# Kernel tuning notes

Measured on AMD Instinct MI355X. Metric: run time of the kernel, lower is better.

## Reference

```python
import jax, jax.numpy as jnp
import numpy as np

INSIZE = 300
OUTSIZE = 300
HSIZE = 300
B, T = 128, 1024


def setup_inputs() -> dict:
    key = jax.random.key(0)
    kx, k1, kb1, k2, kb2 = jax.random.split(key, 5)
    # PyTorch Linear init scale ~ 1/sqrt(fan_in); exact distribution irrelevant for a reference
    s1 = 1.0 / np.sqrt(INSIZE + HSIZE)
    s2 = 1.0 / np.sqrt(HSIZE)
    return {
        "x": jax.random.normal(kx, (B, T, INSIZE), dtype=jnp.float32),
        "W1": jax.random.uniform(k1, (HSIZE, INSIZE + HSIZE), jnp.float32, -s1, s1),
        "b1": jax.random.uniform(kb1, (HSIZE,), jnp.float32, -s1, s1),
        "W2": jax.random.uniform(k2, (OUTSIZE, HSIZE), jnp.float32, -s2, s2),
        "b2": jax.random.uniform(kb2, (OUTSIZE,), jnp.float32, -s2, s2),
    }


def reference(x, W1, b1, W2, b2):
    b = x.shape[0]
    h0 = jnp.zeros((b, HSIZE), dtype=x.dtype)
    # split lin1 weight into input and recurrent parts to avoid per-step concat
    W1x = W1[:, :INSIZE]   # [H, E]
    W1h = W1[:, INSIZE:]   # [H, H]

    def step(h, x_t):
        # h_new = sigmoid(cat([x_t, h]) @ W1.T + b1)
        h_new = jax.nn.sigmoid(x_t @ W1x.T + h @ W1h.T + b1)
        out = h_new @ W2.T + b2
        return h_new, out

    h_final, outs = jax.lax.scan(step, h0, jnp.swapaxes(x, 0, 1))  # outs: [T, B, O]
    return jnp.swapaxes(outs, 0, 1), h_final
```

## Files before the change

### kernel.cpp

```cpp
#include <hip/hip_runtime.h>

typedef __attribute__((ext_vector_type(4))) float f32x4;
typedef __attribute__((ext_vector_type(8))) short bf16x8;

#define B_   128
#define T_   1024
#define NROW 131072
#define HB   (NROW*300)
#define NL2E -1.44269504088896340736f

__device__ inline unsigned short f2bf(float f) {
    union { float f; unsigned int u; } v; v.f = f;
    unsigned int r = v.u + 0x7FFFu + ((v.u >> 16) & 1u);
    return (unsigned short)(r >> 16);
}

__device__ inline uint4 load8_cvt_s(const float* src, bool rowok, int krem, float scale) {
    f32x4 v0 = {0.f,0.f,0.f,0.f}, v1 = {0.f,0.f,0.f,0.f};
    if (rowok) {
        if (krem >= 8)      { v0 = *(const f32x4*)src; v1 = *(const f32x4*)(src + 4); }
        else if (krem >= 4) { v0 = *(const f32x4*)src; }
    }
    v0 *= scale; v1 *= scale;
    uint4 p;
    p.x = (unsigned)f2bf(v0[0]) | ((unsigned)f2bf(v0[1]) << 16);
    p.y = (unsigned)f2bf(v0[2]) | ((unsigned)f2bf(v0[3]) << 16);
    p.z = (unsigned)f2bf(v1[0]) | ((unsigned)f2bf(v1[1]) << 16);
    p.w = (unsigned)f2bf(v1[2]) | ((unsigned)f2bf(v1[3]) << 16);
    return p;
}

__device__ inline uint4 load8_cvt(const float* src, bool rowok, int krem) {
    return load8_cvt_s(src, rowok, krem, 1.0f);
}

__global__ __launch_bounds__(512) void gemm_in_t2(
    const float* __restrict__ X, const float* __restrict__ W1,
    const float* __restrict__ b1, char* __restrict__ aws)
{
    __shared__ unsigned short wlds[19 * 64 * 8];
    __shared__ unsigned short xlds[2][8 * 64 * 8];
    const int tid = threadIdx.x;
    const int w = tid >> 6, l = tid & 63, lg = l >> 4, ln = l & 15;
    const int th = w >> 2, wb = w & 3;
    const int t = blockIdx.x * 2 + th;

    f32x4 acc[2][19];
    #pragma unroll
    for (int q = 0; q < 2; ++q)
        #pragma unroll
        for (int mt = 0; mt < 19; ++mt) acc[q][mt] = (f32x4){0.f,0.f,0.f,0.f};

    for (int kt = 0; kt < 10; ++kt) {
        const int kc = kt * 32;
        __syncthreads();
        #pragma unroll
        for (int rep = 0; rep < 3; ++rep) {
            int e = tid + rep * 512;
            if (e < 1216) {
                int nn = e >> 2, kh = e & 3;
                int k0 = kc + kh * 8;
                uint4 p = load8_cvt_s(W1 + (size_t)nn * 600 + k0, nn < 300, 300 - k0, NL2E);
                *(uint4*)&wlds[(((nn >> 4) * 64) + kh * 16 + (nn & 15)) * 8] = p;
            }
        }
        #pragma unroll
        for (int tt = 0; tt < 2; ++tt) {
            int e = tid;
            int row = e >> 2, kh = e & 3;
            int k0 = kc + kh * 8;
            uint4 p = load8_cvt(X + ((size_t)row * 1024 + blockIdx.x * 2 + tt) * 300 + k0,
                                true, 300 - k0);
            *(uint4*)&xlds[tt][(((row >> 4) * 64) + kh * 16 + (row & 15)) * 8] = p;
        }
        __syncthreads();
        bf16x8 wfr[19];
        #pragma unroll
        for (int mt = 0; mt < 19; ++mt) wfr[mt] = *(const bf16x8*)&wlds[(mt * 64 + l) * 8];
        #pragma unroll
        for (int q = 0; q < 2; ++q) {
            bf16x8 xfr = *(const bf16x8*)&xlds[th][((wb * 2 + q) * 64 + l) * 8];
            #pragma unroll
            for (int mt = 0; mt < 19; ++mt)
                acc[q][mt] = __builtin_amdgcn_mfma_f32_16x16x32_bf16(wfr[mt], xfr, acc[q][mt], 0, 0, 0);
        }
    }

    char* tb = aws + (size_t)t * 76800;
    #pragma unroll
    for (int q = 0; q < 2; ++q) {
        int b = (wb * 2 + q) * 16 + ln;
        #pragma unroll
        for (int mt = 0; mt < 19; ++mt) {
            int rg = mt * 4 + lg;
            if (rg < 75) {
                f32x4 bias = *(const f32x4*)(b1 + mt * 16 + lg * 4);
                float v0 = acc[q][mt][0] + bias[0] * NL2E;
                float v1 = acc[q][mt][1] + bias[1] * NL2E;
                float v2 = acc[q][mt][2] + bias[2] * NL2E;
                float v3 = acc[q][mt][3] + bias[3] * NL2E;
                unsigned plo, phi;
                asm("v_cvt_pk_bf16_f32 %0, %1, %2" : "=v"(plo) : "v"(v0), "v"(v1));
                asm("v_cvt_pk_bf16_f32 %0, %1, %2" : "=v"(phi) : "v"(v2), "v"(v3));
                uint2 pk; pk.x = plo; pk.y = phi;
                *(uint2*)(tb + (size_t)rg * 1024 + b * 8) = pk;
            }
        }
    }
}

#define QOK(q) ((q) < 2 || w4)

#define K2_CHAIN(q)                                                             \
    _Pragma("unroll")                                                           \
    for (int kt = 0; kt < 5; ++kt) {                                            \
        acc[q]  = __builtin_amdgcn_mfma_f32_16x16x32_bf16(afrag[q][kt],   bfr[kt],   acc[q],  0, 0, 0); \
        accB[q] = __builtin_amdgcn_mfma_f32_16x16x32_bf16(afrag[q][kt+5], bfr[kt+5], accB[q], 0, 0, 0); \
    }

#define K2_SIG(q, P, HWT, t)                                                    \
    {                                                                           \
        f32x4 hv;                                                               \
        _Pragma("unroll")                                                       \
        for (int i = 0; i < 4; ++i) {                                           \
            float zn = acc[q][i] + accB[q][i];                  \
            float ex, sg;                                                       \
            asm("v_exp_f32 %0, %1" : "=v"(ex) : "v"(zn));                       \
            asm("v_rcp_f32 %0, %1" : "=v"(sg) : "v"(1.0f + ex));                \
            hv[i] = sg;                                                         \
        }                                                                       \
        unsigned plo, phi;                                                      \
        asm("v_cvt_pk_bf16_f32 %0, %1, %2" : "=v"(plo) : "v"(hv[0]), "v"(hv[1])); \
        asm("v_cvt_pk_bf16_f32 %0, %1, %2" : "=v"(phi) : "v"(hv[2]), "v"(hv[3])); \
        uint2 pk; pk.x = plo; pk.y = phi;                                       \
        *(uint2*)((char*)hlds + ((P) ^ 1) * 10240 + ldsoff[q]) = pk;            \
        if (rq[q] < 300) {                                                      \
            *(uint2*)((HWT) + loff[q]) = pk;         \
            if ((t) == T_ - 1)                                                  \
                *(f32x4*)(hfinal + bb * 300 + rq[q]) = hv;                      \
        }                                                                       \
    }

#define K2W_STEP(P, tval, AS, HWT)                                              \
    {                                                                           \
        const int t = (tval);                                                   \
        bf16x8 bfr[10];                                                         \
        _Pragma("unroll")                                                       \
        for (int kt = 0; kt < 10; ++kt)                                         \
            bfr[kt] = *(const bf16x8*)&hlds[P][(kt * 64 + l) * 8];              \
        f32x4 acc[3], accB[3];                                                  \
        _Pragma("unroll")                                                       \
        for (int q = 0; q < 3; ++q) {                                           \
            union { float f; unsigned u; } u0, u1, u2, u3;                      \
            u0.u = AS[q].x << 16; u1.u = AS[q].x & 0xFFFF0000u;                 \
            u2.u = AS[q].y << 16; u3.u = AS[q].y & 0xFFFF0000u;                 \
            acc[q] = (f32x4){u0.f, u1.f, u2.f, u3.f};                           \
            accB[q] = (f32x4){0.f,0.f,0.f,0.f};                                 \
        }                                                                       \
                        \
        _Pragma("unroll")                                                       \
        for (int q = 0; q < 3; ++q)                                             \
            if (QOK(q)) AS[q] = *(const uint2*)((HWT) + 153600 + loff[q]);      \
        __builtin_amdgcn_s_setprio(1);                                          \
        K2_CHAIN(0)                                                             \
        K2_CHAIN(1)                                                             \
        __builtin_amdgcn_s_setprio(0);                                          \
        K2_SIG(0, P, HWT, t)                                                    \
        if (w4) {                                                               \
            __builtin_amdgcn_s_setprio(1);                                      \
            K2_CHAIN(2)                                                         \
            __builtin_amdgcn_s_setprio(0);                                      \
        }                                                                       \
        K2_SIG(1, P, HWT, t)                                                    \
        if (w4) K2_SIG(2, P, HWT, t)                                            \
        HWT += 153600;                                                          \
        asm volatile("s_waitcnt lgkmcnt(0)" ::: "memory");                      \
        __builtin_amdgcn_s_barrier();                                           \
        asm volatile("" ::: "memory");                                          \
    }

__global__ __launch_bounds__(512) void elman_rec_ws(
    const float* __restrict__ W1, float* __restrict__ hfinal,
    char* __restrict__ hws)
{
    __shared__ unsigned short hlds[2][10 * 64 * 8];
    const int tid = threadIdx.x;
    const int w = tid >> 6, l = tid & 63, lg = l >> 4, ln = l & 15;
    const bool w4 = (w < 4);
    const int bb = blockIdx.x * 16 + ln;

    int rq[3], ldsoff[3], loff[3];
    #pragma unroll
    for (int q = 0; q < 3; ++q) {
        int tile = w4 ? (3 * w + q) : (12 + 2 * (w - 4) + q);
        int r = tile * 16 + 4 * lg;
        rq[q] = r;
        ldsoff[q] = (((r >> 5) * 64 + ((r >> 3) & 3) * 16 + ln) * 8 + (r & 7)) * 2;
        int rgc = r >> 2; if (rgc > 74) rgc = 74;
        loff[q] = rgc * 1024 + bb * 8;
    }

    bf16x8 afrag[3][10];
    #pragma unroll
    for (int q = 0; q < 3; ++q) {
        #pragma unroll
        for (int kt = 0; kt < 10; ++kt) {
            bool qa = (q < 2) || w4;
            int tile = w4 ? (3 * w + q) : (12 + 2 * (w - 4) + q);
            int r = tile * 16 + ln;
            int k0 = kt * 32 + lg * 8;
            uint4 p = load8_cvt_s(W1 + (size_t)r * 600 + 300 + k0,
                                  qa && r < 300, 300 - k0, NL2E);
            union { uint4 u; bf16x8 s; } cv; cv.u = p;
            afrag[q][kt] = cv.s;
        }
    }

    for (int i = tid; i < 10 * 64 * 8; i += 512) hlds[0][i] = 0;

    char* HWT0 = hws;
    char* HWT1 = hws + 76800;

    uint2 AS0[3], AS1[3];
    #pragma unroll
    for (int q = 0; q < 3; ++q)
        if (QOK(q)) {
            AS0[q] = *(const uint2*)(HWT0 + loff[q]);
            AS1[q] = *(const uint2*)(HWT1 + loff[q]);
        }
    __syncthreads();

    for (int t2 = 0; t2 < T_; t2 += 2) {
        K2W_STEP(0, t2,     AS0, HWT0)
        K2W_STEP(1, t2 + 1, AS1, HWT1)
    }
}

__global__ __launch_bounds__(512) void gemm_out_t2(
    const char* __restrict__ hws, const float* __restrict__ W2,
    const float* __restrict__ b2, float* __restrict__ out)
{
    __shared__ unsigned short ahs[2][8 * 132 * 4];
    __shared__ unsigned short blds[19 * 64 * 8];
    const int tid = threadIdx.x;
    const int w = tid >> 6, l = tid & 63, lg = l >> 4, ln = l & 15;
    const int th = w >> 2, wb = w & 3;
    const int t = blockIdx.x * 2 + th;

    f32x4 acc[2][19];
    #pragma unroll
    for (int q = 0; q < 2; ++q)
        #pragma unroll
        for (int nt = 0; nt < 19; ++nt) acc[q][nt] = (f32x4){0.f,0.f,0.f,0.f};

    for (int kt = 0; kt < 10; ++kt) {
        const int kc = kt * 32;
        __syncthreads();
        #pragma unroll
        for (int tt = 0; tt < 2; ++tt) {
            const char* hbase = hws + (size_t)(blockIdx.x * 2 + tt) * 76800;
            #pragma unroll
            for (int it = 0; it < 2; ++it) {
                int e = tid + it * 512;
                int rg = e >> 7, b = e & 127;
                int rgg = kt * 8 + rg;
                uint2 v = make_uint2(0u, 0u);
                if (rgg < 75) v = *(const uint2*)(hbase + (size_t)rgg * 1024 + b * 8);
                *(uint2*)&ahs[tt][(rg * 132 + b) * 4] = v;
            }
        }
        #pragma unroll
        for (int rep = 0; rep < 3; ++rep) {
            int e = tid + rep * 512;
            if (e < 1216) {
                int nn = e >> 2, kh = e & 3;
                int k0 = kc + kh * 8;
                uint4 p = load8_cvt(W2 + (size_t)nn * 300 + k0, nn < 300, 300 - k0);
                *(uint4*)&blds[(((nn >> 4) * 64) + kh * 16 + (nn & 15)) * 8] = p;
            }
        }
        __syncthreads();
        bf16x8 bfr[19];
        #pragma unroll
        for (int nt = 0; nt < 19; ++nt) bfr[nt] = *(const bf16x8*)&blds[(nt * 64 + l) * 8];
        #pragma unroll
        for (int q = 0; q < 2; ++q) {
            int b = (wb * 2 + q) * 16 + ln;
            uint2 u0 = *(const uint2*)&ahs[th][((2 * lg)     * 132 + b) * 4];
            uint2 u1 = *(const uint2*)&ahs[th][((2 * lg + 1) * 132 + b) * 4];
            union { uint4 u; bf16x8 s; } cv;
            cv.u.x = u0.x; cv.u.y = u0.y; cv.u.z = u1.x; cv.u.w = u1.y;
            bf16x8 afr = cv.s;
            #pragma unroll
            for (int nt = 0; nt < 19; ++nt)
                acc[q][nt] = __builtin_amdgcn_mfma_f32_16x16x32_bf16(afr, bfr[nt], acc[q][nt], 0, 0, 0);
        }
    }

    #pragma unroll
    for (int q = 0; q < 2; ++q)
        #pragma unroll
        for (int nt = 0; nt < 19; ++nt) {
            int n = nt * 16 + ln;
            if (n < 300) {
                float bias = b2[n];
                int b0r = (wb * 2 + q) * 16 + lg * 4;
                #pragma unroll
                for (int i = 0; i < 4; ++i)
                    out[((size_t)(b0r + i) * T_ + t) * 300 + n] = acc[q][nt][i] + bias;
            }
        }
}

__global__ __launch_bounds__(256) void gemm_in(
    const float* __restrict__ X, const float* __restrict__ W1,
    const float* __restrict__ b1, float* __restrict__ A)
{
    __shared__ unsigned short alds[8 * 64 * 8];
    __shared__ unsigned short blds[10 * 64 * 8];
    const int tid = threadIdx.x;
    const int w = tid >> 6, l = tid & 63, lg = l >> 4, ln = l & 15;
    const size_t m0 = (size_t)blockIdx.x * 128;
    const int n0 = blockIdx.y * 160;

    f32x4 acc[2][10];
    #pragma unroll
    for (int q = 0; q < 2; ++q)
        #pragma unroll
        for (int nt = 0; nt < 10; ++nt) acc[q][nt] = (f32x4){0.f,0.f,0.f,0.f};

    for (int kt = 0; kt < 10; ++kt) {
        const int kc = kt * 32;
        __syncthreads();
        #pragma unroll
        for (int rep = 0; rep < 2; ++rep) {
            int e = tid + rep * 256;
            int row = e >> 2, kh = e & 3;
            int k0 = kc + kh * 8;
            uint4 p = load8_cvt(X + (m0 + row) * 300 + k0, true, 300 - k0);
            *(uint4*)&alds[(((row >> 4) * 64) + kh * 16 + (row & 15)) * 8] = p;
        }
        #pragma unroll
        for (int rep = 0; rep < 3; ++rep) {
            int e = tid + rep * 256;
            if (e < 640) {
                int nn = e >> 2, kh = e & 3;
                int n = n0 + nn;
                int k0 = kc + kh * 8;
                uint4 p = load8_cvt(W1 + (size_t)n * 600 + k0, n < 300, 300 - k0);
                *(uint4*)&blds[(((nn >> 4) * 64) + kh * 16 + (nn & 15)) * 8] = p;
            }
        }
        __syncthreads();
        bf16x8 bfr[10];
        #pragma unroll
        for (int nt = 0; nt < 10; ++nt) bfr[nt] = *(const bf16x8*)&blds[(nt * 64 + l) * 8];
        #pragma unroll
        for (int q = 0; q < 2; ++q) {
            bf16x8 afr = *(const bf16x8*)&alds[((w * 2 + q) * 64 + l) * 8];
            #pragma unroll
            for (int nt = 0; nt < 10; ++nt)
                acc[q][nt] = __builtin_amdgcn_mfma_f32_16x16x32_bf16(afr, bfr[nt], acc[q][nt], 0, 0, 0);
        }
    }

    #pragma unroll
    for (int q = 0; q < 2; ++q)
        #pragma unroll
        for (int nt = 0; nt < 10; ++nt) {
            int n = n0 + nt * 16 + ln;
            if (n < 300) {
                float bias = b1[n];
                size_t mr = m0 + (w * 2 + q) * 16 + lg * 4;
                #pragma unroll
                for (int i = 0; i < 4; ++i)
                    A[(mr + i) * 300 + n] = (acc[q][nt][i] + bias) * NL2E;
            }
        }
}

#define K2_STEP(P, tval, ASLOT, APTR, HPME, HPOTHER)                            \
    {                                                                           \
        const int t = (tval);                                                   \
        const int tt = t - 1;                                                   \
        const size_t so = (size_t)(tt >> 6) * 76800 + (size_t)(tt & 63) * 600;  \
        bf16x8 bfr[10];                                                         \
        _Pragma("unroll")                                                       \
        for (int kt = 0; kt < 10; ++kt)                                         \
            bfr[kt] = *(const bf16x8*)&hlds[P][(kt * 64 + l) * 8];              \
        f32x4 acc[3], accB[3];                                                  \
        _Pragma("unroll")                                                       \
        for (int q = 0; q < 3; ++q) {                                           \
            acc[q] = QOK(q) ? ASLOT[q] : (f32x4){0.f,0.f,0.f,0.f};              \
            accB[q] = (f32x4){0.f,0.f,0.f,0.f};                                 \
        }                                                                       \
        _Pragma("unroll")                                                       \
        for (int q = 0; q < 3; ++q)                                             \
            if (QOK(q)) ASLOT[q] = *(const f32x4*)(APTR + rq[q] * 4);           \
        APTR += 2400;                                                           \
        __builtin_amdgcn_s_setprio(1);                                          \
        _Pragma("unroll")                                                       \
        for (int kt = 0; kt < 5; ++kt) {                                        \
            acc[0]  = __builtin_amdgcn_mfma_f32_16x16x32_bf16(afrag[0][kt],   bfr[kt],   acc[0],  0, 0, 0); \
            accB[0] = __builtin_amdgcn_mfma_f32_16x16x32_bf16(afrag[0][kt+5], bfr[kt+5], accB[0], 0, 0, 0); \
            acc[1]  = __builtin_amdgcn_mfma_f32_16x16x32_bf16(afrag[1][kt],   bfr[kt],   acc[1],  0, 0, 0); \
            accB[1] = __builtin_amdgcn_mfma_f32_16x16x32_bf16(afrag[1][kt+5], bfr[kt+5], accB[1], 0, 0, 0); \
            if (w4) {                                                           \
                acc[2]  = __builtin_amdgcn_mfma_f32_16x16x32_bf16(afrag[2][kt],   bfr[kt],   acc[2],  0, 0, 0); \
                accB[2] = __builtin_amdgcn_mfma_f32_16x16x32_bf16(afrag[2][kt+5], bfr[kt+5], accB[2], 0, 0, 0); \
            }                                                                   \
        }                                                                       \
        __builtin_amdgcn_s_setprio(0);                                          \
        _Pragma("unroll")                                                       \
        for (int q = 0; q < 3; ++q) {                                           \
            if (!QOK(q)) continue;                                              \
            f32x4 hv;                                                           \
            _Pragma("unroll")                                                   \
            for (int i = 0; i < 4; ++i) {                                       \
                float zn = acc[q][i] + accB[q][i];                              \
                float ex, sg;                                                   \
                asm("v_exp_f32 %0, %1" : "=v"(ex) : "v"(zn));                   \
                asm("v_rcp_f32 %0, %1" : "=v"(sg) : "v"(1.0f + ex));            \
                hv[i] = sg;                                                     \
            }                                                                   \
            unsigned plo, phi;                                                  \
            asm("v_cvt_pk_bf16_f32 %0, %1, %2" : "=v"(plo) : "v"(hv[0]), "v"(hv[1])); \
            asm("v_cvt_pk_bf16_f32 %0, %1, %2" : "=v"(phi) : "v"(hv[2]), "v"(hv[3])); \
            HPME[q].x = plo; HPME[q].y = phi;                                   \
            *(uint2*)((char*)hlds + ((P) ^ 1) * 10240 + ldsoff[q]) = HPME[q];   \
            if (t > 0 && rq[q] < 300)                                           \
                *(uint2*)(sbase + so + rq[q] * 2) = HPOTHER[q];                 \
        }                                                                       \
        asm volatile("s_waitcnt lgkmcnt(0)" ::: "memory");                      \
        __builtin_amdgcn_s_barrier();                                           \
        asm volatile("" ::: "memory");                                          \
    }

__global__ __launch_bounds__(512) void elman_rec_mfma(
    const float* __restrict__ W1, float* __restrict__ buf,
    float* __restrict__ hfinal)
{
    __shared__ unsigned short hlds[2][10 * 64 * 8];
    const int tid = threadIdx.x;
    const int w = tid >> 6, l = tid & 63, lg = l >> 4, ln = l & 15;
    const bool w4 = (w < 4);
    const int bb = blockIdx.x * 16 + ln;

    int rq[3], ldsoff[3];
    #pragma unroll
    for (int q = 0; q < 3; ++q) {
        int tile = w4 ? (3 * w + q) : (12 + 2 * (w - 4) + q);
        int r = tile * 16 + 4 * lg;
        rq[q] = r;
        ldsoff[q] = (((r >> 5) * 64 + ((r >> 3) & 3) * 16 + ln) * 8 + (r & 7)) * 2;
    }

    bf16x8 afrag[3][10];
    #pragma unroll
    for (int q = 0; q < 3; ++q) {
        #pragma unroll
        for (int kt = 0; kt < 10; ++kt) {
            bool qa = (q < 2) || w4;
            int tile = w4 ? (3 * w + q) : (12 + 2 * (w - 4) + q);
            int r = tile * 16 + ln;
            int k0 = kt * 32 + lg * 8;
            uint4 p = load8_cvt_s(W1 + (size_t)r * 600 + 300 + k0,
                                  qa && r < 300, 300 - k0, NL2E);
            union { uint4 u; bf16x8 s; } cv; cv.u = p;
            afrag[q][kt] = cv.s;
        }
    }

    for (int i = tid; i < 10 * 64 * 8; i += 512) hlds[0][i] = 0;

    const char* abase = (const char*)(buf + (size_t)bb * T_ * 300);
    char* sbase = (char*)buf + (size_t)bb * 16 * 76800;

    f32x4 A0[3], A1[3];
    #pragma unroll
    for (int q = 0; q < 3; ++q)
        if (QOK(q)) {
            A0[q] = *(const f32x4*)(abase + rq[q] * 4);
            A1[q] = *(const f32x4*)(abase + 1200 + rq[q] * 4);
        }
    const char* aptr0 = abase + 2400;
    const char* aptr1 = abase + 3600;
    uint2 hpA[3], hpB[3];
    __syncthreads();

    for (int t2 = 0; t2 < T_; t2 += 2) {
        K2_STEP(0, t2,     A0, aptr0, hpA, hpB)
        K2_STEP(1, t2 + 1, A1, aptr1, hpB, hpA)
    }

    {
        const int tt = T_ - 1;
        const size_t so = (size_t)(tt >> 6) * 76800 + (size_t)(tt & 63) * 600;
        #pragma unroll
        for (int q = 0; q < 3; ++q)
            if (QOK(q) && rq[q] < 300) {
                *(uint2*)(sbase + so + rq[q] * 2) = hpB[q];
                f32x4 hv;
                union { float f; unsigned u; } c0, c1, c2, c3;
                c0.u = hpB[q].x << 16; c1.u = hpB[q].x & 0xFFFF0000u;
                c2.u = hpB[q].y << 16; c3.u = hpB[q].y & 0xFFFF0000u;
                hv[0] = c0.f; hv[1] = c1.f; hv[2] = c2.f; hv[3] = c3.f;
                *(f32x4*)(hfinal + bb * 300 + rq[q]) = hv;
            }
    }
}

__global__ __launch_bounds__(256) void gemm_out(
    float* __restrict__ buf, const float* __restrict__ W2,
    const float* __restrict__ b2)
{
    __shared__ unsigned short alds[4 * 64 * 8];
    __shared__ unsigned short blds[19 * 64 * 8];
    const int tid = threadIdx.x;
    const int w = tid >> 6, l = tid & 63, lg = l >> 4, ln = l & 15;
    const size_t chunk = blockIdx.x;
    const char* pbase = (const char*)buf + chunk * 76800;

    f32x4 acc[19];
    #pragma unroll
    for (int nt = 0; nt < 19; ++nt) acc[nt] = (f32x4){0.f,0.f,0.f,0.f};

    for (int kt = 0; kt < 10; ++kt) {
        const int kc = kt * 32;
        __syncthreads();
        {
            int row = tid >> 2, kh = tid & 3;
            int k0 = kc + kh * 8;
            const char* p = pbase + row * 600;
            uint2 lo = make_uint2(0u, 0u), hi = make_uint2(0u, 0u);
            int krem = 300 - k0;
            if (krem >= 8)      { lo = *(const uint2*)(p + k0 * 2); hi = *(const uint2*)(p + k0 * 2 + 8); }
            else if (krem >= 4) { lo = *(const uint2*)(p + k0 * 2); }
            uint4 pk; pk.x = lo.x; pk.y = lo.y; pk.z = hi.x; pk.w = hi.y;
            *(uint4*)&alds[(((row >> 4) * 64) + kh * 16 + (row & 15)) * 8] = pk;
        }
        #pragma unroll
        for (int rep = 0; rep < 5; ++rep) {
            int e = tid + rep * 256;
            if (e < 1216) {
                int nn = e >> 2, kh = e & 3;
                int k0 = kc + kh * 8;
                uint4 p = load8_cvt(W2 + (size_t)nn * 300 + k0, nn < 300, 300 - k0);
                *(uint4*)&blds[(((nn >> 4) * 64) + kh * 16 + (nn & 15)) * 8] = p;
            }
        }
        __syncthreads();
        bf16x8 afr = *(const bf16x8*)&alds[(w * 64 + l) * 8];
        #pragma unroll
        for (int nt = 0; nt < 19; ++nt) {
            bf16x8 bfr = *(const bf16x8*)&blds[(nt * 64 + l) * 8];
            acc[nt] = __builtin_amdgcn_mfma_f32_16x16x32_bf16(afr, bfr, acc[nt], 0, 0, 0);
        }
    }

    float* frow = buf + chunk * 19200;
    #pragma unroll
    for (int nt = 0; nt < 19; ++nt) {
        int n = nt * 16 + ln;
        if (n < 300) {
            float bias = b2[n];
            int mr = w * 16 + lg * 4;
            #pragma unroll
            for (int i = 0; i < 4; ++i)
                frow[(mr + i) * 300 + n] = acc[nt][i] + bias;
        }
    }
}

extern "C" void kernel_launch(void* const* d_in, const int* in_sizes, int n_in,
                              void* d_out, int out_size, void* d_ws, size_t ws_size,
                              hipStream_t stream)
{
    const float* x  = (const float*)d_in[0];
    const float* W1 = (const float*)d_in[1];
    const float* b1 = (const float*)d_in[2];
    const float* W2 = (const float*)d_in[3];
    const float* b2 = (const float*)d_in[4];

    float* out    = (float*)d_out;
    float* hfinal = out + (size_t)HB;

    const size_t HT4 = (size_t)T_ * 75 * 128 * 8;
    if (ws_size >= HT4 + 2 * 76800) {
        gemm_in_t2<<<512, 512, 0, stream>>>(x, W1, b1, (char*)d_ws);
        elman_rec_ws<<<8, 512, 0, stream>>>(W1, hfinal, (char*)d_ws);
        gemm_out_t2<<<512, 512, 0, stream>>>((const char*)d_ws, W2, b2, out);
    } else {
        gemm_in<<<dim3(1024, 2), 256, 0, stream>>>(x, W1, b1, out);
        elman_rec_mfma<<<8, 512, 0, stream>>>(W1, out, hfinal);
        gemm_out<<<2048, 256, 0, stream>>>(out, W2, b2);
    }
}
```

Measured before the change: 992.1 us.

## Split recurrent K loop in halves and defer upper-half sigmoid across steps

```diff
diff --git a/kernel.cpp b/kernel.cpp
--- a/kernel.cpp
+++ b/kernel.cpp
@@ -109,45 +109,37 @@
     }
 }
 
-#define QOK(q) ((q) < 2 || w4)
-
-#define K2_CHAIN(q)                                                             \
-    _Pragma("unroll")                                                           \
-    for (int kt = 0; kt < 5; ++kt) {                                            \
-        acc[q]  = __builtin_amdgcn_mfma_f32_16x16x32_bf16(afrag[q][kt],   bfr[kt],   acc[q],  0, 0, 0); \
-        accB[q] = __builtin_amdgcn_mfma_f32_16x16x32_bf16(afrag[q][kt+5], bfr[kt+5], accB[q], 0, 0, 0); \
-    }
-
-#define K2_SIG(q, P, HWT, t)                                                    \
-    {                                                                           \
-        f32x4 hv;                                                               \
+#define QK2(q) ((q) < 2 || lo3)
+
+#define SIG4(zin)                                                               \
+        f32x4 hv; uint2 pk;                                                     \
         _Pragma("unroll")                                                       \
         for (int i = 0; i < 4; ++i) {                                           \
-            float zn = acc[q][i] + accB[q][i];                  \
             float ex, sg;                                                       \
-            asm("v_exp_f32 %0, %1" : "=v"(ex) : "v"(zn));                       \
+            asm("v_exp_f32 %0, %1" : "=v"(ex) : "v"(zin[i]));                   \
             asm("v_rcp_f32 %0, %1" : "=v"(sg) : "v"(1.0f + ex));                \
             hv[i] = sg;                                                         \
         }                                                                       \
-        unsigned plo, phi;                                                      \
-        asm("v_cvt_pk_bf16_f32 %0, %1, %2" : "=v"(plo) : "v"(hv[0]), "v"(hv[1])); \
-        asm("v_cvt_pk_bf16_f32 %0, %1, %2" : "=v"(phi) : "v"(hv[2]), "v"(hv[3])); \
-        uint2 pk; pk.x = plo; pk.y = phi;                                       \
-        *(uint2*)((char*)hlds + ((P) ^ 1) * 10240 + ldsoff[q]) = pk;            \
-        if (rq[q] < 300) {                                                      \
-            *(uint2*)((HWT) + loff[q]) = pk;         \
-            if ((t) == T_ - 1)                                                  \
-                *(f32x4*)(hfinal + bb * 300 + rq[q]) = hv;                      \
-        }                                                                       \
-    }
-
-#define K2W_STEP(P, tval, AS, HWT)                                              \
+        asm("v_cvt_pk_bf16_f32 %0, %1, %2" : "=v"(pk.x) : "v"(hv[0]), "v"(hv[1])); \
+        asm("v_cvt_pk_bf16_f32 %0, %1, %2" : "=v"(pk.y) : "v"(hv[2]), "v"(hv[3]));
+
+#define K2S(RB, tval, AS, FIRST)                                                \
     {                                                                           \
         const int t = (tval);                                                   \
-        bf16x8 bfr[10];                                                         \
-        _Pragma("unroll")                                                       \
-        for (int kt = 0; kt < 10; ++kt)                                         \
-            bfr[kt] = *(const bf16x8*)&hlds[P][(kt * 64 + l) * 8];              \
+              \
+        if (g_up && !(FIRST)) {                                                 \
+            _Pragma("unroll")                                                   \
+            for (int q = 0; q < 3; ++q) {                                       \
+                if (!QK2(q)) continue;                                          \
+                SIG4(uacc[q])                                                   \
+                *(uint2*)((char*)hlds + (RB) * 10240 + ldsoff[q]) = pk;         \
+                if (rq[q] < 300) *(uint2*)(UPT + loff[q]) = pk;                 \
+            }                                                                   \
+        }                                                                       \
+        bf16x8 bfr[5];                                                          \
+        _Pragma("unroll")                                                       \
+        for (int kt = 0; kt < 5; ++kt)                                          \
+            bfr[kt] = *(const bf16x8*)&hlds[RB][(kt * 64 + l) * 8];             \
         f32x4 acc[3], accB[3];                                                  \
         _Pragma("unroll")                                                       \
         for (int q = 0; q < 3; ++q) {                                           \
@@ -155,27 +147,74 @@
             u0.u = AS[q].x << 16; u1.u = AS[q].x & 0xFFFF0000u;                 \
             u2.u = AS[q].y << 16; u3.u = AS[q].y & 0xFFFF0000u;                 \
             acc[q] = (f32x4){u0.f, u1.f, u2.f, u3.f};                           \
-            accB[q] = (f32x4){0.f,0.f,0.f,0.f};                                 \
-        }                                                                       \
-                        \
+            accB[q] = (f32x4){0.f, 0.f, 0.f, 0.f};                              \
+        }                                                                       \
+                                                          \
         _Pragma("unroll")                                                       \
         for (int q = 0; q < 3; ++q)                                             \
-            if (QOK(q)) AS[q] = *(const uint2*)((HWT) + 153600 + loff[q]);      \
+            if (QK2(q)) AS[q] = *(const uint2*)(LWT + 153600 + loff[q]);        \
         __builtin_amdgcn_s_setprio(1);                                          \
-        K2_CHAIN(0)                                                             \
-        K2_CHAIN(1)                                                             \
+        _Pragma("unroll")                                                       \
+        for (int kt = 0; kt < 3; ++kt) {                                        \
+            acc[0] = __builtin_amdgcn_mfma_f32_16x16x32_bf16(afrag[0][kt], bfr[kt], acc[0], 0, 0, 0); \
+            acc[1] = __builtin_amdgcn_mfma_f32_16x16x32_bf16(afrag[1][kt], bfr[kt], acc[1], 0, 0, 0); \
+            if (lo3)                                                            \
+                acc[2] = __builtin_amdgcn_mfma_f32_16x16x32_bf16(afrag[2][kt], bfr[kt], acc[2], 0, 0, 0); \
+        }                                                                       \
+        _Pragma("unroll")                                                       \
+        for (int kt = 3; kt < 5; ++kt) {                                        \
+            accB[0] = __builtin_amdgcn_mfma_f32_16x16x32_bf16(afrag[0][kt], bfr[kt], accB[0], 0, 0, 0); \
+            accB[1] = __builtin_amdgcn_mfma_f32_16x16x32_bf16(afrag[1][kt], bfr[kt], accB[1], 0, 0, 0); \
+            if (lo3)                                                            \
+                accB[2] = __builtin_amdgcn_mfma_f32_16x16x32_bf16(afrag[2][kt], bfr[kt], accB[2], 0, 0, 0); \
+        }                                                                       \
         __builtin_amdgcn_s_setprio(0);                                          \
-        K2_SIG(0, P, HWT, t)                                                    \
-        if (w4) {                                                               \
-            __builtin_amdgcn_s_setprio(1);                                      \
-            K2_CHAIN(2)                                                         \
-            __builtin_amdgcn_s_setprio(0);                                      \
-        }                                                                       \
-        K2_SIG(1, P, HWT, t)                                                    \
-        if (w4) K2_SIG(2, P, HWT, t)                                            \
-        HWT += 153600;                                                          \
         asm volatile("s_waitcnt lgkmcnt(0)" ::: "memory");                      \
-        __builtin_amdgcn_s_barrier();                                           \
+        __builtin_amdgcn_s_barrier();          \
+        asm volatile("" ::: "memory");                                          \
+        _Pragma("unroll")                                                       \
+        for (int kt = 0; kt < 5; ++kt)                                          \
+            bfr[kt] = *(const bf16x8*)&hlds[RB][((kt + 5) * 64 + l) * 8];       \
+        __builtin_amdgcn_s_setprio(1);                                          \
+        _Pragma("unroll")                                                       \
+        for (int kt = 0; kt < 3; ++kt) {                                        \
+            acc[0] = __builtin_amdgcn_mfma_f32_16x16x32_bf16(afrag[0][kt + 5], bfr[kt], acc[0], 0, 0, 0); \
+            acc[1] = __builtin_amdgcn_mfma_f32_16x16x32_bf16(afrag[1][kt + 5], bfr[kt], acc[1], 0, 0, 0); \
+            if (lo3)                                                            \
+                acc[2] = __builtin_amdgcn_mfma_f32_16x16x32_bf16(afrag[2][kt + 5], bfr[kt], acc[2], 0, 0, 0); \
+        }                                                                       \
+        _Pragma("unroll")                                                       \
+        for (int kt = 3; kt < 5; ++kt) {                                        \
+            accB[0] = __builtin_amdgcn_mfma_f32_16x16x32_bf16(afrag[0][kt + 5], bfr[kt], accB[0], 0, 0, 0); \
+            accB[1] = __builtin_amdgcn_mfma_f32_16x16x32_bf16(afrag[1][kt + 5], bfr[kt], accB[1], 0, 0, 0); \
+            if (lo3)                                                            \
+                accB[2] = __builtin_amdgcn_mfma_f32_16x16x32_bf16(afrag[2][kt + 5], bfr[kt], accB[2], 0, 0, 0); \
+        }                                                                       \
+        __builtin_amdgcn_s_setprio(0);                                          \
+        if (!g_up) {                                                            \
+            _Pragma("unroll")                                                   \
+            for (int q = 0; q < 3; ++q) {                                       \
+                if (!QK2(q)) continue;                                          \
+                f32x4 z;                                                        \
+                _Pragma("unroll")                                               \
+                for (int i = 0; i < 4; ++i) z[i] = acc[q][i] + accB[q][i];      \
+                SIG4(z)                                                         \
+                *(uint2*)((char*)hlds + ((RB) ^ 1) * 10240 + ldsoff[q]) = pk;   \
+                *(uint2*)(LWT + loff[q]) = pk;        \
+                if (t == T_ - 1)                                                \
+                    *(f32x4*)(hfinal + bb * 300 + rq[q]) = hv;                  \
+            }                                                                   \
+        } else {                                                                \
+            _Pragma("unroll")                                                   \
+            for (int q = 0; q < 3; ++q) {                                       \
+                if (!QK2(q)) continue;                                          \
+                _Pragma("unroll")                                               \
+                for (int i = 0; i < 4; ++i) uacc[q][i] = acc[q][i] + accB[q][i]; \
+            }                                                                   \
+        }                                                                       \
+        LWT += 76800; UPT += 76800;                                             \
+        asm volatile("s_waitcnt lgkmcnt(0)" ::: "memory");                      \
+        __builtin_amdgcn_s_barrier();            \
         asm volatile("" ::: "memory");                                          \
     }
 
@@ -186,14 +225,16 @@
     __shared__ unsigned short hlds[2][10 * 64 * 8];
     const int tid = threadIdx.x;
     const int w = tid >> 6, l = tid & 63, lg = l >> 4, ln = l & 15;
-    const bool w4 = (w < 4);
+    const int g_up = w >> 2;
+    const int wl = w & 3;
+    const bool lo3 = (wl < 2);
+    const int tbase = g_up * 10 + (lo3 ? wl * 3 : 6 + (wl - 2) * 2);
     const int bb = blockIdx.x * 16 + ln;
 
     int rq[3], ldsoff[3], loff[3];
     #pragma unroll
     for (int q = 0; q < 3; ++q) {
-        int tile = w4 ? (3 * w + q) : (12 + 2 * (w - 4) + q);
-        int r = tile * 16 + 4 * lg;
+        int r = (tbase + q) * 16 + 4 * lg;
         rq[q] = r;
         ldsoff[q] = (((r >> 5) * 64 + ((r >> 3) & 3) * 16 + ln) * 8 + (r & 7)) * 2;
         int rgc = r >> 2; if (rgc > 74) rgc = 74;
@@ -205,9 +246,8 @@
     for (int q = 0; q < 3; ++q) {
         #pragma unroll
         for (int kt = 0; kt < 10; ++kt) {
-            bool qa = (q < 2) || w4;
-            int tile = w4 ? (3 * w + q) : (12 + 2 * (w - 4) + q);
-            int r = tile * 16 + ln;
+            bool qa = QK2(q);
+            int r = (tbase + q) * 16 + ln;
             int k0 = kt * 32 + lg * 8;
             uint4 p = load8_cvt_s(W1 + (size_t)r * 600 + 300 + k0,
                                   qa && r < 300, 300 - k0, NL2E);
@@ -218,21 +258,38 @@
 
     for (int i = tid; i < 10 * 64 * 8; i += 512) hlds[0][i] = 0;
 
-    char* HWT0 = hws;
-    char* HWT1 = hws + 76800;
+    char* LWT = hws;
+    char* UPT = hws - 76800;
 
     uint2 AS0[3], AS1[3];
-    #pragma unroll
-    for (int q = 0; q < 3; ++q)
-        if (QOK(q)) {
-            AS0[q] = *(const uint2*)(HWT0 + loff[q]);
-            AS1[q] = *(const uint2*)(HWT1 + loff[q]);
-        }
+    f32x4 uacc[3];
+    #pragma unroll
+    for (int q = 0; q < 3; ++q) {
+        uacc[q] = (f32x4){0.f,0.f,0.f,0.f};
+        if (QK2(q)) {
+            AS0[q] = *(const uint2*)(hws + loff[q]);
+            AS1[q] = *(const uint2*)(hws + 76800 + loff[q]);
+        }
+    }
     __syncthreads();
 
-    for (int t2 = 0; t2 < T_; t2 += 2) {
-        K2W_STEP(0, t2,     AS0, HWT0)
-        K2W_STEP(1, t2 + 1, AS1, HWT1)
+    K2S(0, 0, AS0, true)
+    for (int t2 = 1; t2 < 1023; t2 += 2) {
+        K2S(1, t2,     AS1, false)
+        K2S(0, t2 + 1, AS0, false)
+    }
+    K2S(1, 1023, AS1, false)
+
+    if (g_up) {
+        #pragma unroll
+        for (int q = 0; q < 3; ++q) {
+            if (!QK2(q)) continue;
+            SIG4(uacc[q])
+            if (rq[q] < 300) {
+                *(uint2*)(UPT + loff[q]) = pk;
+                *(f32x4*)(hfinal + bb * 300 + rq[q]) = hv;
+            }
+        }
     }
 }
 
@@ -311,6 +368,8 @@
             }
         }
 }
+
+#define QOK(q) ((q) < 2 || w4)
 
 __global__ __launch_bounds__(256) void gemm_in(
     const float* __restrict__ X, const float* __restrict__ W1,
```

Result: slower. 1.295 ms (+30.5%).
